# Kernel tuning notes

Hardware: AMD Instinct MI355X
Metric: run time of the kernel (lower is better)

## Reference

```python
import jax, jax.numpy as jnp
import numpy as np

B, N, M, K = 4, 16384, 16384, 16   # batch, points, centers, neighbors
C, O, G = 64, 64, 8                # in_planes, out_planes, group


def setup_inputs() -> dict:
    key = jax.random.key(0)
    ks = jax.random.split(key, 16)
    r = lambda i, sh, s=1.0: jax.random.normal(ks[i], sh, jnp.float32) * s
    return dict(
        center_pos=r(0, (B, M, 3)),
        center_fea=r(1, (B, C, M)),
        pos=r(2, (B, N, 3)),
        fea=r(3, (B, C, N)),
        idx=jax.random.randint(ks[4], (B, M, K), 0, N, jnp.int32),
        # linear q/k/v
        Wq=r(5, (C, O), 0.05), bq=jnp.zeros((O,), jnp.float32),
        Wk=r(6, (C, O), 0.05), bk=jnp.zeros((O,), jnp.float32),
        Wv=r(7, (C, O), 0.05), bv=jnp.zeros((O,), jnp.float32),
        # center_pos_encode: conv1x1(3->O, no bias) + folded BN (scale,shift) + relu + conv1x1(O->O)
        cpe_w1=r(8, (3, O), 0.05), cpe_s=jnp.ones((O,), jnp.float32), cpe_b=jnp.zeros((O,), jnp.float32),
        cpe_w2=r(9, (O, O), 0.05), cpe_b2=jnp.zeros((O,), jnp.float32),
        # pos_encode (Conv2d 1x1 == per-point linear)
        pe_w1=r(10, (3, O), 0.05), pe_s=jnp.ones((O,), jnp.float32), pe_b=jnp.zeros((O,), jnp.float32),
        pe_w2=r(11, (O, O), 0.05), pe_b2=jnp.zeros((O,), jnp.float32),
        # weight_encode (O -> G)
        we_w1=r(12, (O, G), 0.05), we_s=jnp.ones((G,), jnp.float32), we_b=jnp.zeros((G,), jnp.float32),
        we_w2=r(13, (G, G), 0.05), we_b2=jnp.zeros((G,), jnp.float32),
    )


def _mlp2(x, w1, s, b, w2, b2):
    # conv1x1(no bias) -> inference BatchNorm folded to (scale, shift) -> ReLU -> conv1x1(+bias)
    h = jax.nn.relu(x @ w1 * s + b)
    return h @ w2 + b2


def reference(center_pos, center_fea, pos, fea, idx,
              Wq, bq, Wk, bk, Wv, bv,
              cpe_w1, cpe_s, cpe_b, cpe_w2, cpe_b2,
              pe_w1, pe_s, pe_b, pe_w2, pe_b2,
              we_w1, we_s, we_b, we_w2, we_b2):
    x_q = center_fea.transpose(0, 2, 1) @ Wq + bq        # [B,M,O]
    ft = fea.transpose(0, 2, 1)                          # [B,N,C]
    x_k = ft @ Wk + bk                                   # [B,N,O]
    x_v = ft @ Wv + bv                                   # [B,N,O]

    gather = jax.vmap(lambda a, i: a[i])                 # per-batch irregular gather
    nk = gather(x_k, idx)                                # [B,M,K,O]
    nv = gather(x_v, idx)                                # [B,M,K,O]
    npos = gather(pos, idx) - center_pos[:, :, None, :]  # [B,M,K,3] relative coords

    cpr = _mlp2(center_pos, cpe_w1, cpe_s, cpe_b, cpe_w2, cpe_b2)  # [B,M,O]
    pr = _mlp2(npos, pe_w1, pe_s, pe_b, pe_w2, pe_b2)              # [B,M,K,O]

    r_qk = nk - x_q[:, :, None, :] + cpr[:, :, None, :]  # [B,M,K,O]
    v = nv + pr                                          # [B,M,K,O]

    w = _mlp2(r_qk, we_w1, we_s, we_b, we_w2, we_b2)     # [B,M,K,G]
    w = jax.nn.softmax(w, axis=2)                        # softmax over neighbors

    v = v.reshape(B, M, K, G, O // G)
    out = jnp.einsum('bmkgi,bmkg->bmgi', v, w).reshape(B, M, O)
    return out.transpose(0, 2, 1)                        # [B,O,M]
```

## Files before the change

### kernel.cpp

```cpp
#include <hip/hip_runtime.h>
#include <hip/hip_bf16.h>

typedef unsigned short u16;
typedef __attribute__((ext_vector_type(8))) __bf16 bf8v;
typedef __attribute__((ext_vector_type(4))) float f32x4;
typedef __attribute__((ext_vector_type(4))) unsigned uint4v;

#define B_ 4
#define N_ 16384
#define M_ 16384
#define K_ 16
#define C_ 64
#define O_ 64
#define G_ 8

__device__ __forceinline__ float bf2f(u16 x){
  union { unsigned u; float f; } v; v.u = ((unsigned)x) << 16; return v.f;
}
__device__ __forceinline__ u16 f2bf(float f){
  union { float f; unsigned u; } v; v.f = f;
  unsigned u = v.u;
  return (u16)((u + 0x7FFFu + ((u >> 16) & 1u)) >> 16);
}
union pk2 { unsigned u; _Float16 h[2]; };
__device__ __forceinline__ unsigned packh(float a, float b){
  pk2 p; p.h[0] = (_Float16)a; p.h[1] = (_Float16)b; return p.u;
}

__global__ __launch_bounds__(256) void setup_kernel(
    const float* __restrict__ Wq, const float* __restrict__ bq,
    const float* __restrict__ cpe_w2, const float* __restrict__ cpe_b2,
    const float* __restrict__ we_w1,
    const float* __restrict__ Wk, const float* __restrict__ bk,
    const float* __restrict__ Wv, const float* __restrict__ bv,
    const float* __restrict__ cpe_w1, const float* __restrict__ cpe_s, const float* __restrict__ cpe_b,
    u16* __restrict__ bw, float* __restrict__ cinit,
    u16* __restrict__ wkv, float* __restrict__ bias, float* __restrict__ cpe)
{
  __shared__ float sWe[512];
  int tid = threadIdx.x;
  for (int e = tid; e < 512; e += 256) sWe[e] = we_w1[e];
  __syncthreads();
  {
    int k = tid >> 1, g0 = (tid & 1)*4;
    const float* brow = (k < 64) ? (cpe_w2 + k*64) : (Wq + (k-64)*64);
    float sgn = (k < 64) ? 1.f : -1.f;
    float aw[4] = {0.f,0.f,0.f,0.f};
    for (int o = 0; o < 64; o++){
      float bo = brow[o]*sgn;
      #pragma unroll
      for (int gg=0; gg<4; gg++) aw[gg] += bo * sWe[o*8 + g0+gg];
    }
    #pragma unroll
    for (int gg=0; gg<4; gg++) bw[(g0+gg)*136 + k] = f2bf(aw[gg]);
  }
  for (int e = tid; e < 2176; e += 256){
    int r = e / 136, cc = e % 136;
    if (r >= 8 || cc >= 128) bw[e] = 0;
  }
  if (tid < 8){
    float s = 0.f;
    for (int o = 0; o < 64; o++) s += (cpe_b2[o] - bq[o]) * sWe[o*8 + tid];
    cinit[tid] = s;
  }
  for (int e = tid; e < 9216; e += 256){
    int col = e / 72, k = e - col*72;
    float v = 0.f;
    if (k < 64) v = (col < 64) ? Wk[k*64 + col] : Wv[k*64 + (col-64)];
    wkv[e] = f2bf(v);
  }
  if (tid < 128) bias[tid] = (tid < 64) ? bk[tid] : bv[tid-64];
  if (tid < 64){
    float sc = cpe_s[tid];
    cpe[tid]      = cpe_w1[tid]*sc;
    cpe[64+tid]   = cpe_w1[64+tid]*sc;
    cpe[128+tid]  = cpe_w1[128+tid]*sc;
    cpe[192+tid]  = cpe_b[tid];
  }
}

__global__ __launch_bounds__(256) void pre_kernel(
    const float* __restrict__ center_pos, const float* __restrict__ center_fea,
    const float* __restrict__ fea,
    const u16* __restrict__ bw, const float* __restrict__ cinit,
    const u16* __restrict__ wkv, const float* __restrict__ bias, const float* __restrict__ cpe,
    u16* __restrict__ xk, u16* __restrict__ xv, float* __restrict__ qw)
{
  __shared__ u16 sWT[128*72];
  __shared__ u16 sA[64*72];
  __shared__ u16 sOut[64*136];
  __shared__ float sMisc[256];
  int tid = threadIdx.x;
  int l = tid & 63, w = tid >> 6, c = l & 15, q = l >> 4;
  int blk = blockIdx.x;

  if (blk < 256){
    int P0 = blk * 256; int b = P0 >> 14; int n00 = P0 & (N_-1);
    const float* fb = fea + (long)b*C_*N_;
    for (int e = tid; e < 1152; e += 256)
      ((uint4v*)sWT)[e] = ((const uint4v*)wkv)[e];
    if (tid < 128) sMisc[tid] = bias[tid];

    #pragma unroll 1
    for (int s = 0; s < 4; s++){
      int n0 = n00 + s*64;
      #pragma unroll
      for (int pp = 0; pp < 4; pp++){
        int k = pp*16 + (tid >> 4);
        int nf = (tid & 15)*4;
        f32x4 v = *(const f32x4*)&fb[(long)k*N_ + n0 + nf];
        sA[(nf+0)*72+k] = f2bf(v[0]); sA[(nf+1)*72+k] = f2bf(v[1]);
        sA[(nf+2)*72+k] = f2bf(v[2]); sA[(nf+3)*72+k] = f2bf(v[3]);
      }
      __syncthreads();

      bf8v af0 = *(const bf8v*)&sA[(w*16+c)*72 + q*8];
      bf8v af1 = *(const bf8v*)&sA[(w*16+c)*72 + 32 + q*8];
      f32x4 acc[8];
      #pragma unroll
      for (int t = 0; t < 8; t++){
        float bb = sMisc[16*t + c];
        f32x4 a_ = {bb, bb, bb, bb};
        bf8v b0 = *(const bf8v*)&sWT[(16*t + c)*72 + q*8];
        bf8v b1 = *(const bf8v*)&sWT[(16*t + c)*72 + 32 + q*8];
        a_ = __builtin_amdgcn_mfma_f32_16x16x32_bf16(af0, b0, a_, 0,0,0);
        a_ = __builtin_amdgcn_mfma_f32_16x16x32_bf16(af1, b1, a_, 0,0,0);
        acc[t] = a_;
      }
      #pragma unroll
      for (int t = 0; t < 8; t++)
        #pragma unroll
        for (int r = 0; r < 4; r++)
          sOut[(w*16 + q*4 + r)*136 + 16*t + c] = f2bf(acc[t][r]);
      __syncthreads();

      #pragma unroll
      for (int rep = 0; rep < 4; rep++){
        int chunk = rep*256 + tid;
        int pt = chunk >> 4, c8i = chunk & 15;
        uint4v val = *(const uint4v*)&sOut[pt*136 + c8i*8];
        int col8 = c8i*8;
        long row = (long)P0 + s*64 + pt;
        if (col8 < 64) *(uint4v*)(xk + row*64 + col8)      = val;
        else           *(uint4v*)(xv + row*64 + (col8-64)) = val;
      }
      __syncthreads();
    }
  } else {
    int P0 = (blk - 256) * 256; int b = P0 >> 14; int m00 = P0 & (M_-1);
    const float* cfb = center_fea + (long)b*C_*M_;
    float* sQ = (float*)sOut;
    for (int e = tid; e < 272; e += 256)
      ((uint4v*)sWT)[e] = ((const uint4v*)bw)[e];
    if (tid < 256) sMisc[tid] = cpe[tid];

    #pragma unroll 1
    for (int s = 0; s < 4; s++){
      int m0 = m00 + s*64;
      #pragma unroll
      for (int pp = 0; pp < 4; pp++){
        int k = pp*16 + (tid >> 4);
        int nf = (tid & 15)*4;
        f32x4 v = *(const f32x4*)&cfb[(long)k*M_ + m0 + nf];
        sA[(nf+0)*72+k] = f2bf(v[0]); sA[(nf+1)*72+k] = f2bf(v[1]);
        sA[(nf+2)*72+k] = f2bf(v[2]); sA[(nf+3)*72+k] = f2bf(v[3]);
      }
      long c3 = (long)(P0 + s*64 + w*16 + c)*3;
      float cp0 = center_pos[c3], cp1 = center_pos[c3+1], cp2 = center_pos[c3+2];
      __syncthreads();

      bf8v ah[2];
      #pragma unroll
      for (int ks = 0; ks < 2; ks++){
        union { bf8v v; u16 sv[8]; } ua;
        #pragma unroll
        for (int j = 0; j < 8; j++){
          int h = ks*32 + q*8 + j;
          float hv = cp0*sMisc[h] + cp1*sMisc[64+h] + cp2*sMisc[128+h] + sMisc[192+h];
          ua.sv[j] = f2bf(fmaxf(hv, 0.f));
        }
        ah[ks] = ua.v;
      }
      bf8v acf0 = *(const bf8v*)&sA[(w*16+c)*72 + q*8];
      bf8v acf1 = *(const bf8v*)&sA[(w*16+c)*72 + 32 + q*8];

      float ci = (c < 8) ? cinit[c] : 0.f;
      f32x4 aq = {ci, ci, ci, ci};
      {
        bf8v b0 = *(const bf8v*)&sWT[c*136 + q*8];
        bf8v b1 = *(const bf8v*)&sWT[c*136 + 32 + q*8];
        bf8v b2 = *(const bf8v*)&sWT[c*136 + 64 + q*8];
        bf8v b3 = *(const bf8v*)&sWT[c*136 + 96 + q*8];
        aq = __builtin_amdgcn_mfma_f32_16x16x32_bf16(ah[0], b0, aq, 0,0,0);
        aq = __builtin_amdgcn_mfma_f32_16x16x32_bf16(ah[1], b1, aq, 0,0,0);
        aq = __builtin_amdgcn_mfma_f32_16x16x32_bf16(acf0,  b2, aq, 0,0,0);
        aq = __builtin_amdgcn_mfma_f32_16x16x32_bf16(acf1,  b3, aq, 0,0,0);
      }
      __syncthreads();
      if (c < 8){
        #pragma unroll
        for (int r = 0; r < 4; r++) sQ[(w*16 + q*4 + r)*8 + c] = aq[r];
      }
      __syncthreads();
      for (int e = tid; e < 512; e += 256)
        qw[(long)(P0 + s*64)*8 + e] = sQ[e];
      __syncthreads();
    }
  }
}

__global__ __launch_bounds__(256) void attn_kernel(
    const float* __restrict__ center_pos, const float* __restrict__ pos,
    const int* __restrict__ idx,
    const float* __restrict__ pe_w1, const float* __restrict__ pe_s, const float* __restrict__ pe_b,
    const float* __restrict__ pe_w2, const float* __restrict__ pe_b2,
    const float* __restrict__ we_w1, const float* __restrict__ we_s, const float* __restrict__ we_b,
    const float* __restrict__ we_w2, const float* __restrict__ we_b2,
    const u16* __restrict__ xk, const u16* __restrict__ xv, const float* __restrict__ qw,
    float* __restrict__ out)
{
  int tid = threadIdx.x;
  __shared__ float s_w1f[192], s_pb[64], s_pb2[64], s_ww2[64];
  __shared__ float s_ws8[8], s_wb8[8], s_wb28[8];
  __shared__ f32x4 s_dyn4[1232];
  __shared__ float s_tile[32*66];

  char* dynb = (char*)s_dyn4;

  if (tid < 64){
    float sc = pe_s[tid];
    s_w1f[tid]     = pe_w1[tid]*sc;
    s_w1f[64+tid]  = pe_w1[64+tid]*sc;
    s_w1f[128+tid] = pe_w1[128+tid]*sc;
    s_pb[tid]  = pe_b[tid];
    s_pb2[tid] = pe_b2[tid];
    s_ww2[tid] = we_w2[tid];
  }
  if (tid >= 64 && tid < 72){
    int g = tid-64;
    s_ws8[g]=we_s[g]; s_wb8[g]=we_b[g]; s_wb28[g]=we_b2[g];
  }
  u16* stg = (u16*)dynb;
  #pragma unroll
  for (int pp = 0; pp < 4; pp++){
    int row = pp*16 + (tid >> 4);
    int colf = (tid & 15)*4;
    f32x4 v = *(const f32x4*)&pe_w2[row*64 + colf];
    stg[(colf+0)*72+row] = f2bf(v[0]); stg[(colf+1)*72+row] = f2bf(v[1]);
    stg[(colf+2)*72+row] = f2bf(v[2]); stg[(colf+3)*72+row] = f2bf(v[3]);
  }
  u16* stg2 = (u16*)(dynb + 9216);
  for (int e = tid; e < 512; e += 256){
    int k = e >> 3, cc = e & 7;
    stg2[cc*72 + k] = f2bf(we_w1[e]);
  }
  for (int e = tid; e < 576; e += 256) stg2[576 + e] = 0;
  __syncthreads();

  int w = tid >> 6, l = tid & 63, c = l & 15, q = l >> 4, c8 = c & 7, qb = l & 48;

  bf8v pw2f[4][2], ww1f[2], w2B;
  #pragma unroll
  for (int t = 0; t < 4; t++){
    pw2f[t][0] = *(const bf8v*)&stg[(t*16+c)*72 + q*8];
    pw2f[t][1] = *(const bf8v*)&stg[(t*16+c)*72 + 32 + q*8];
  }
  ww1f[0] = *(const bf8v*)&stg2[c*72 + q*8];
  ww1f[1] = *(const bf8v*)&stg2[c*72 + 32 + q*8];
  {
    union { bf8v v; u16 s[8]; } uu;
    #pragma unroll
    for (int j = 0; j < 8; j++)
      uu.s[j] = (q == 0 && c < 8) ? f2bf(s_ww2[j*8 + c]) : (u16)0;
    w2B = uu.v;
  }
  float ws_c = s_ws8[c8], wb_c = s_wb8[c8], wb2_c = s_wb28[c8];
  float pb2l = s_pb2[l];
  __syncthreads();

  float* sv  = (float*)(dynb + w*4928);
  u16*  swt  = (u16*) (dynb + w*4928 + 4352);
  u16*  sh   = (u16*) (dynb + w*4928 + 4672);

  int pbase = blockIdx.x * 32;
  int b = pbase >> 14;
  long xkb = (long)b * N_ * 64;
  int ch = c >> 3;
  int gl = (l >> 3) & 7;

  int p = pbase + w*8;
  int iv = idx[(long)p*16 + c];
  float qpv = qw[(long)p*8 + c8];
  long c30 = (long)p*3;
  float cp0 = center_pos[c30], cp1 = center_pos[c30+1], cp2 = center_pos[c30+2];
  long pr30 = ((long)b*N_ + iv) * 3;
  float px = pos[pr30], py = pos[pr30+1], pz = pos[pr30+2];
  const u16* krow0 = xk + xkb + (long)iv * 64;
  bf8v ka0 = *(const bf8v*)(krow0 + q*8);
  bf8v ka1 = *(const bf8v*)(krow0 + 32 + q*8);
  const u16* vrow0 = xv + xkb + (long)iv * 64;
  uint4v va0 = *(const uint4v*)(vrow0 + q*8);
  uint4v va1 = *(const uint4v*)(vrow0 + 32 + q*8);

  #pragma unroll 1
  for (int i = 0; i < 8; i++){
    int pn = p + ((i < 7) ? 1 : 0);
    int iv_n = idx[(long)pn*16 + c];
    float qpv_n = qw[(long)pn*8 + c8];
    long c3n = (long)pn*3;
    float cpn0 = center_pos[c3n], cpn1 = center_pos[c3n+1], cpn2 = center_pos[c3n+2];
    long pr3n = ((long)b*N_ + iv_n) * 3;
    float pxn = pos[pr3n], pyn = pos[pr3n+1], pzn = pos[pr3n+2];
    const u16* krn = xk + xkb + (long)iv_n * 64;
    bf8v kan0 = *(const bf8v*)(krn + q*8);
    bf8v kan1 = *(const bf8v*)(krn + 32 + q*8);
    const u16* vrn = xv + xkb + (long)iv_n * 64;
    uint4v van0 = *(const uint4v*)(vrn + q*8);
    uint4v van1 = *(const uint4v*)(vrn + 32 + q*8);

    {
      union { uint4v u; u16 s[8]; } A0, A1;
      A0.u = va0; A1.u = va1;
      f32x4 vf0, vf1, vf2, vf3;
      #pragma unroll
      for (int jj = 0; jj < 4; jj++){
        vf0[jj] = bf2f(A0.s[jj]);   vf1[jj] = bf2f(A0.s[4+jj]);
        vf2[jj] = bf2f(A1.s[jj]);   vf3[jj] = bf2f(A1.s[4+jj]);
      }
      f32x4* d0 = (f32x4*)&sv[c*68 + q*8];
      d0[0] = vf0; d0[1] = vf1;
      f32x4* d1 = (f32x4*)&sv[c*68 + 32 + q*8];
      d1[0] = vf2; d1[1] = vf3;
    }

    float np0 = px - cp0, np1 = py - cp1, np2 = pz - cp2;
    bf8v h1f[2];
    #pragma unroll
    for (int ks = 0; ks < 2; ks++){
      union { bf8v v; u16 s[8]; } hu;
      #pragma unroll
      for (int j = 0; j < 8; j++){
        int o = ks*32 + q*8 + j;
        float hv = np0*s_w1f[o] + np1*s_w1f[64+o] + np2*s_w1f[128+o] + s_pb[o];
        hu.s[j] = f2bf(fmaxf(hv, 0.f));
      }
      h1f[ks] = hu.v;
    }

    f32x4 h2a = {qpv, qpv, qpv, qpv};
    h2a = __builtin_amdgcn_mfma_f32_16x16x32_bf16(ka0, ww1f[0], h2a, 0,0,0);
    h2a = __builtin_amdgcn_mfma_f32_16x16x32_bf16(ka1, ww1f[1], h2a, 0,0,0);

    if (c < 8){
      #pragma unroll
      for (int r = 0; r < 4; r++)
        sh[(q*4+r)*8 + c] = f2bf(fmaxf(h2a[r]*ws_c + wb_c, 0.f));
    }
    bf8v hrow = *(const bf8v*)&sh[c*8];
    bf8v zf; { union { bf8v v; u16 s[8]; } uz;
      #pragma unroll
      for (int j=0;j<8;j++) uz.s[j]=0; zf = uz.v; }
    bf8v ahf = (q == 0) ? hrow : zf;

    f32x4 wlv = {wb2_c, wb2_c, wb2_c, wb2_c};
    wlv = __builtin_amdgcn_mfma_f32_16x16x32_bf16(ahf, w2B, wlv, 0,0,0);

    float e0 = exp2f(wlv[0]*1.44269504f);
    float e1 = exp2f(wlv[1]*1.44269504f);
    float e2 = exp2f(wlv[2]*1.44269504f);
    float e3 = exp2f(wlv[3]*1.44269504f);
    float sm = e0+e1+e2+e3;
    sm += __shfl_xor(sm, 16, 64);
    sm += __shfl_xor(sm, 32, 64);
    float rn = 1.0f / sm;
    e0 *= rn; e1 *= rn; e2 *= rn; e3 *= rn;
    unsigned ep0 = packh(e0, e1), ep1 = packh(e2, e3);

    if (c < 8){
      *(unsigned*)&swt[c*20 + q*4]     = ep0;
      *(unsigned*)&swt[c*20 + q*4 + 2] = ep1;
    }

    float ov[4];
    #pragma unroll
    for (int t = 0; t < 4; t++){
      f32x4 z = {0.f,0.f,0.f,0.f};
      z = __builtin_amdgcn_mfma_f32_16x16x32_bf16(h1f[0], pw2f[t][0], z, 0,0,0);
      z = __builtin_amdgcn_mfma_f32_16x16x32_bf16(h1f[1], pw2f[t][1], z, 0,0,0);
      int src = qb | (t*2 + ch);
      pk2 wA; wA.u = (unsigned)__shfl((int)ep0, src, 64);
      pk2 wB; wB.u = (unsigned)__shfl((int)ep1, src, 64);
      ov[t] = z[0]*(float)wA.h[0] + z[1]*(float)wA.h[1]
            + z[2]*(float)wB.h[0] + z[3]*(float)wB.h[1];
    }
    #pragma unroll
    for (int t = 0; t < 4; t++){
      ov[t] += __shfl_xor(ov[t], 16, 64);
      ov[t] += __shfl_xor(ov[t], 32, 64);
    }
    float ovsel = ov[0];
    ovsel = (q==1) ? ov[1] : ovsel;
    ovsel = (q==2) ? ov[2] : ovsel;
    ovsel = (q==3) ? ov[3] : ovsel;

    float acc = 0.f;
    {
      const unsigned* wr = (const unsigned*)&swt[gl*20];
      #pragma unroll
      for (int k2 = 0; k2 < 8; k2++){
        pk2 wp; wp.u = wr[k2];
        acc += sv[(2*k2)*68 + l]   * (float)wp.h[0];
        acc += sv[(2*k2+1)*68 + l] * (float)wp.h[1];
      }
    }

    s_tile[(w*8+i)*66 + l] = ovsel + acc + pb2l;

    p = pn; iv = iv_n; qpv = qpv_n;
    cp0 = cpn0; cp1 = cpn1; cp2 = cpn2;
    px = pxn; py = pyn; pz = pzn;
    ka0 = kan0; ka1 = kan1; va0 = van0; va1 = van1;
  }
  __syncthreads();

  int o0 = tid >> 5, pt = tid & 31;
  int m0 = pbase & (M_-1);
  long outb = ((long)b*64) * M_ + m0 + pt;
  #pragma unroll
  for (int ii = 0; ii < 8; ii++){
    int o = o0*8 + ii;
    out[outb + (long)o*M_] = s_tile[pt*66 + o];
  }
}

extern "C" void kernel_launch(void* const* d_in, const int* in_sizes, int n_in,
                              void* d_out, int out_size, void* d_ws, size_t ws_size,
                              hipStream_t stream) {
  const float* center_pos = (const float*)d_in[0];
  const float* center_fea = (const float*)d_in[1];
  const float* pos        = (const float*)d_in[2];
  const float* fea        = (const float*)d_in[3];
  const int*   idx        = (const int*)d_in[4];
  const float* Wq = (const float*)d_in[5];   const float* bq = (const float*)d_in[6];
  const float* Wk = (const float*)d_in[7];   const float* bk = (const float*)d_in[8];
  const float* Wv = (const float*)d_in[9];   const float* bv = (const float*)d_in[10];
  const float* cpe_w1 = (const float*)d_in[11]; const float* cpe_s = (const float*)d_in[12];
  const float* cpe_b  = (const float*)d_in[13]; const float* cpe_w2 = (const float*)d_in[14];
  const float* cpe_b2 = (const float*)d_in[15];
  const float* pe_w1 = (const float*)d_in[16]; const float* pe_s = (const float*)d_in[17];
  const float* pe_b  = (const float*)d_in[18]; const float* pe_w2 = (const float*)d_in[19];
  const float* pe_b2 = (const float*)d_in[20];
  const float* we_w1 = (const float*)d_in[21]; const float* we_s = (const float*)d_in[22];
  const float* we_b  = (const float*)d_in[23]; const float* we_w2 = (const float*)d_in[24];
  const float* we_b2 = (const float*)d_in[25];

  const size_t SZ = (size_t)B_*N_*64;
  u16* xk = (u16*)d_ws;
  u16* xv = xk + SZ;
  float* qwp = (float*)(xv + SZ);
  u16* bwp = (u16*)(qwp + (size_t)B_*M_*8);
  float* cinitp = (float*)(bwp + 2176);
  u16* wkvp = (u16*)(cinitp + 8);
  float* biasp = (float*)(wkvp + 9216);
  float* cpep = biasp + 128;
  float* outp = (float*)d_out;

  hipLaunchKernelGGL(setup_kernel, dim3(1), dim3(256), 0, stream,
      Wq, bq, cpe_w2, cpe_b2, we_w1, Wk, bk, Wv, bv,
      cpe_w1, cpe_s, cpe_b, bwp, cinitp, wkvp, biasp, cpep);
  hipLaunchKernelGGL(pre_kernel, dim3(512), dim3(256), 0, stream,
      center_pos, center_fea, fea, bwp, cinitp, wkvp, biasp, cpep,
      xk, xv, qwp);
  hipLaunchKernelGGL(attn_kernel, dim3(2048), dim3(256), 0, stream,
      center_pos, pos, idx, pe_w1, pe_s, pe_b, pe_w2, pe_b2,
      we_w1, we_s, we_b, we_w2, we_b2, xk, xv, qwp, outp);
}
```

Before: 229.1 us.

## Fold setup into pre kernel, pad positions to float4, use f16 packed math

Removes the single-block setup kernel and has each pre_kernel block compute its weight transforms (Wk/Wv transpose, folded query/center weights) directly into shared memory. It also writes float4-padded copies of pos and center_pos so the attention kernel can gather positions with one vector load. The attention kernel switches the position-encoding MLP to packed f16 arithmetic and f16 MFMA, and stores softmax weights as f32 in LDS instead of broadcasting them through shuffles. The cost is redundant per-block weight setup, extra LDS and workspace traffic, and different numerical precision in the f16 path.

Result: faster. 207.7 us (-9.3%).

```diff
diff --git a/kernel.cpp b/kernel.cpp
--- a/kernel.cpp
+++ b/kernel.cpp
@@ -3,6 +3,8 @@
 
 typedef unsigned short u16;
 typedef __attribute__((ext_vector_type(8))) __bf16 bf8v;
+typedef __attribute__((ext_vector_type(8))) _Float16 f16x8;
+typedef __attribute__((ext_vector_type(2))) _Float16 h2v;
 typedef __attribute__((ext_vector_type(4))) float f32x4;
 typedef __attribute__((ext_vector_type(4))) unsigned uint4v;
 
@@ -22,74 +24,30 @@
   unsigned u = v.u;
   return (u16)((u + 0x7FFFu + ((u >> 16) & 1u)) >> 16);
 }
-union pk2 { unsigned u; _Float16 h[2]; };
-__device__ __forceinline__ unsigned packh(float a, float b){
-  pk2 p; p.h[0] = (_Float16)a; p.h[1] = (_Float16)b; return p.u;
-}
-
-__global__ __launch_bounds__(256) void setup_kernel(
+__device__ __forceinline__ u16 f2h(float f){
+  union { _Float16 h; u16 u; } v; v.h = (_Float16)f; return v.u;
+}
+__device__ __forceinline__ h2v mkh2(float a, float b){
+  h2v r = {(_Float16)a, (_Float16)b}; return r;
+}
+
+__global__ __launch_bounds__(256) void pre_kernel(
+    const float* __restrict__ center_pos, const float* __restrict__ center_fea,
+    const float* __restrict__ pos, const float* __restrict__ fea,
     const float* __restrict__ Wq, const float* __restrict__ bq,
-    const float* __restrict__ cpe_w2, const float* __restrict__ cpe_b2,
-    const float* __restrict__ we_w1,
     const float* __restrict__ Wk, const float* __restrict__ bk,
     const float* __restrict__ Wv, const float* __restrict__ bv,
     const float* __restrict__ cpe_w1, const float* __restrict__ cpe_s, const float* __restrict__ cpe_b,
-    u16* __restrict__ bw, float* __restrict__ cinit,
-    u16* __restrict__ wkv, float* __restrict__ bias, float* __restrict__ cpe)
-{
-  __shared__ float sWe[512];
-  int tid = threadIdx.x;
-  for (int e = tid; e < 512; e += 256) sWe[e] = we_w1[e];
-  __syncthreads();
-  {
-    int k = tid >> 1, g0 = (tid & 1)*4;
-    const float* brow = (k < 64) ? (cpe_w2 + k*64) : (Wq + (k-64)*64);
-    float sgn = (k < 64) ? 1.f : -1.f;
-    float aw[4] = {0.f,0.f,0.f,0.f};
-    for (int o = 0; o < 64; o++){
-      float bo = brow[o]*sgn;
-      #pragma unroll
-      for (int gg=0; gg<4; gg++) aw[gg] += bo * sWe[o*8 + g0+gg];
-    }
-    #pragma unroll
-    for (int gg=0; gg<4; gg++) bw[(g0+gg)*136 + k] = f2bf(aw[gg]);
-  }
-  for (int e = tid; e < 2176; e += 256){
-    int r = e / 136, cc = e % 136;
-    if (r >= 8 || cc >= 128) bw[e] = 0;
-  }
-  if (tid < 8){
-    float s = 0.f;
-    for (int o = 0; o < 64; o++) s += (cpe_b2[o] - bq[o]) * sWe[o*8 + tid];
-    cinit[tid] = s;
-  }
-  for (int e = tid; e < 9216; e += 256){
-    int col = e / 72, k = e - col*72;
-    float v = 0.f;
-    if (k < 64) v = (col < 64) ? Wk[k*64 + col] : Wv[k*64 + (col-64)];
-    wkv[e] = f2bf(v);
-  }
-  if (tid < 128) bias[tid] = (tid < 64) ? bk[tid] : bv[tid-64];
-  if (tid < 64){
-    float sc = cpe_s[tid];
-    cpe[tid]      = cpe_w1[tid]*sc;
-    cpe[64+tid]   = cpe_w1[64+tid]*sc;
-    cpe[128+tid]  = cpe_w1[128+tid]*sc;
-    cpe[192+tid]  = cpe_b[tid];
-  }
-}
-
-__global__ __launch_bounds__(256) void pre_kernel(
-    const float* __restrict__ center_pos, const float* __restrict__ center_fea,
-    const float* __restrict__ fea,
-    const u16* __restrict__ bw, const float* __restrict__ cinit,
-    const u16* __restrict__ wkv, const float* __restrict__ bias, const float* __restrict__ cpe,
-    u16* __restrict__ xk, u16* __restrict__ xv, float* __restrict__ qw)
+    const float* __restrict__ cpe_w2, const float* __restrict__ cpe_b2,
+    const float* __restrict__ we_w1,
+    u16* __restrict__ xk, u16* __restrict__ xv, float* __restrict__ qw,
+    float* __restrict__ pos4, float* __restrict__ cp4)
 {
   __shared__ u16 sWT[128*72];
   __shared__ u16 sA[64*72];
   __shared__ u16 sOut[64*136];
   __shared__ float sMisc[256];
+  __shared__ float sCi[8];
   int tid = threadIdx.x;
   int l = tid & 63, w = tid >> 6, c = l & 15, q = l >> 4;
   int blk = blockIdx.x;
@@ -97,9 +55,17 @@
   if (blk < 256){
     int P0 = blk * 256; int b = P0 >> 14; int n00 = P0 & (N_-1);
     const float* fb = fea + (long)b*C_*N_;
-    for (int e = tid; e < 1152; e += 256)
-      ((uint4v*)sWT)[e] = ((const uint4v*)wkv)[e];
-    if (tid < 128) sMisc[tid] = bias[tid];
+    for (int e = tid; e < 8192; e += 256){
+      int k = e >> 7, col = e & 127;
+      float v = (col < 64) ? Wk[k*64 + col] : Wv[k*64 + (col-64)];
+      sWT[col*72 + k] = f2bf(v);
+    }
+    if (tid < 128) sMisc[tid] = (tid < 64) ? bk[tid] : bv[tid-64];
+    {
+      long pg = (long)P0 + tid;
+      f32x4 r = {pos[pg*3], pos[pg*3+1], pos[pg*3+2], 0.f};
+      ((f32x4*)pos4)[pg] = r;
+    }
 
     #pragma unroll 1
     for (int s = 0; s < 4; s++){
@@ -149,10 +115,45 @@
   } else {
     int P0 = (blk - 256) * 256; int b = P0 >> 14; int m00 = P0 & (M_-1);
     const float* cfb = center_fea + (long)b*C_*M_;
-    float* sQ = (float*)sOut;
-    for (int e = tid; e < 272; e += 256)
-      ((uint4v*)sWT)[e] = ((const uint4v*)bw)[e];
-    if (tid < 256) sMisc[tid] = cpe[tid];
+    float* sWe = (float*)sOut;
+    float* sQ  = (float*)sOut;
+    for (int e = tid; e < 512; e += 256) sWe[e] = we_w1[e];
+    if (tid < 64){
+      float sc = cpe_s[tid];
+      sMisc[tid]     = cpe_w1[tid]*sc;
+      sMisc[64+tid]  = cpe_w1[64+tid]*sc;
+      sMisc[128+tid] = cpe_w1[128+tid]*sc;
+      sMisc[192+tid] = cpe_b[tid];
+    }
+    {
+      long pg = (long)P0 + tid;
+      f32x4 r = {center_pos[pg*3], center_pos[pg*3+1], center_pos[pg*3+2], 0.f};
+      ((f32x4*)cp4)[pg] = r;
+    }
+    __syncthreads();
+    {
+      int k = tid >> 1, g0 = (tid & 1)*4;
+      const float* brow = (k < 64) ? (cpe_w2 + k*64) : (Wq + (k-64)*64);
+      float sgn = (k < 64) ? 1.f : -1.f;
+      float aw[4] = {0.f,0.f,0.f,0.f};
+      for (int o = 0; o < 64; o++){
+        float bo = brow[o]*sgn;
+        #pragma unroll
+        for (int gg=0; gg<4; gg++) aw[gg] += bo * sWe[o*8 + g0+gg];
+      }
+      #pragma unroll
+      for (int gg=0; gg<4; gg++) sWT[(g0+gg)*136 + k] = f2bf(aw[gg]);
+    }
+    for (int e = tid; e < 2176; e += 256){
+      int r = e / 136, cc = e % 136;
+      if (r >= 8 || cc >= 128) sWT[e] = 0;
+    }
+    if (tid < 8){
+      float s = 0.f;
+      for (int o = 0; o < 64; o++) s += (cpe_b2[o] - bq[o]) * sWe[o*8 + tid];
+      sCi[tid] = s;
+    }
+    __syncthreads();
 
     #pragma unroll 1
     for (int s = 0; s < 4; s++){
@@ -184,7 +185,7 @@
       bf8v acf0 = *(const bf8v*)&sA[(w*16+c)*72 + q*8];
       bf8v acf1 = *(const bf8v*)&sA[(w*16+c)*72 + 32 + q*8];
 
-      float ci = (c < 8) ? cinit[c] : 0.f;
+      float ci = (c < 8) ? sCi[c] : 0.f;
       f32x4 aq = {ci, ci, ci, ci};
       {
         bf8v b0 = *(const bf8v*)&sWT[c*136 + q*8];
@@ -210,7 +211,7 @@
 }
 
 __global__ __launch_bounds__(256) void attn_kernel(
-    const float* __restrict__ center_pos, const float* __restrict__ pos,
+    const float* __restrict__ cp4, const float* __restrict__ pos4,
     const int* __restrict__ idx,
     const float* __restrict__ pe_w1, const float* __restrict__ pe_s, const float* __restrict__ pe_b,
     const float* __restrict__ pe_w2, const float* __restrict__ pe_b2,
@@ -222,7 +223,7 @@
   int tid = threadIdx.x;
   __shared__ float s_w1f[192], s_pb[64], s_pb2[64], s_ww2[64];
   __shared__ float s_ws8[8], s_wb8[8], s_wb28[8];
-  __shared__ f32x4 s_dyn4[1232];
+  __shared__ f32x4 s_dyn4[1312];
   __shared__ float s_tile[32*66];
 
   char* dynb = (char*)s_dyn4;
@@ -246,8 +247,8 @@
     int row = pp*16 + (tid >> 4);
     int colf = (tid & 15)*4;
     f32x4 v = *(const f32x4*)&pe_w2[row*64 + colf];
-    stg[(colf+0)*72+row] = f2bf(v[0]); stg[(colf+1)*72+row] = f2bf(v[1]);
-    stg[(colf+2)*72+row] = f2bf(v[2]); stg[(colf+3)*72+row] = f2bf(v[3]);
+    stg[(colf+0)*72+row] = f2h(v[0]); stg[(colf+1)*72+row] = f2h(v[1]);
+    stg[(colf+2)*72+row] = f2h(v[2]); stg[(colf+3)*72+row] = f2h(v[3]);
   }
   u16* stg2 = (u16*)(dynb + 9216);
   for (int e = tid; e < 512; e += 256){
@@ -259,90 +260,119 @@
 
   int w = tid >> 6, l = tid & 63, c = l & 15, q = l >> 4, c8 = c & 7, qb = l & 48;
 
-  bf8v pw2f[4][2], ww1f[2], w2B;
+  f16x8 pw2f[4][2];
+  bf8v ww1f[2];
+  f16x8 w2B, hz8;
   #pragma unroll
   for (int t = 0; t < 4; t++){
-    pw2f[t][0] = *(const bf8v*)&stg[(t*16+c)*72 + q*8];
-    pw2f[t][1] = *(const bf8v*)&stg[(t*16+c)*72 + 32 + q*8];
+    pw2f[t][0] = *(const f16x8*)&stg[(t*16+c)*72 + q*8];
+    pw2f[t][1] = *(const f16x8*)&stg[(t*16+c)*72 + 32 + q*8];
   }
   ww1f[0] = *(const bf8v*)&stg2[c*72 + q*8];
   ww1f[1] = *(const bf8v*)&stg2[c*72 + 32 + q*8];
   {
-    union { bf8v v; u16 s[8]; } uu;
+    union { f16x8 v; u16 s[8]; } uu;
     #pragma unroll
     for (int j = 0; j < 8; j++)
-      uu.s[j] = (q == 0 && c < 8) ? f2bf(s_ww2[j*8 + c]) : (u16)0;
+      uu.s[j] = (q == 0 && c < 8) ? f2h(s_ww2[j*8 + c]) : (u16)0;
     w2B = uu.v;
-  }
+    #pragma unroll
+    for (int j = 0; j < 8; j++) uu.s[j] = 0;
+    hz8 = uu.v;
+  }
+  h2v cw0[2][4], cw1[2][4], cw2[2][4], cb[2][4];
+  #pragma unroll
+  for (int ks = 0; ks < 2; ks++)
+    #pragma unroll
+    for (int jj = 0; jj < 4; jj++){
+      int o = ks*32 + q*8 + jj*2;
+      cw0[ks][jj] = mkh2(s_w1f[o],     s_w1f[o+1]);
+      cw1[ks][jj] = mkh2(s_w1f[64+o],  s_w1f[65+o]);
+      cw2[ks][jj] = mkh2(s_w1f[128+o], s_w1f[129+o]);
+      cb [ks][jj] = mkh2(s_pb[o],      s_pb[o+1]);
+    }
   float ws_c = s_ws8[c8], wb_c = s_wb8[c8], wb2_c = s_wb28[c8];
   float pb2l = s_pb2[l];
+  h2v hz2 = {(_Float16)0.f, (_Float16)0.f};
   __syncthreads();
 
-  float* sv  = (float*)(dynb + w*4928);
-  u16*  swt  = (u16*) (dynb + w*4928 + 4352);
-  u16*  sh   = (u16*) (dynb + w*4928 + 4672);
+  float* sv  = (float*)(dynb + w*5248);
+  float* swt = (float*)(dynb + w*5248 + 4352);
+  u16*  sh   = (u16*) (dynb + w*5248 + 4992);
 
   int pbase = blockIdx.x * 32;
   int b = pbase >> 14;
-  long xkb = (long)b * N_ * 64;
+  const u16* xkb = xk + (long)b * N_ * 64;
+  const u16* xvb = xv + (long)b * N_ * 64;
+  const f32x4* pos4b = ((const f32x4*)pos4) + (long)b * N_;
   int ch = c >> 3;
-  int gl = (l >> 3) & 7;
-
-  int p = pbase + w*8;
-  int iv = idx[(long)p*16 + c];
-  float qpv = qw[(long)p*8 + c8];
-  long c30 = (long)p*3;
-  float cp0 = center_pos[c30], cp1 = center_pos[c30+1], cp2 = center_pos[c30+2];
-  long pr30 = ((long)b*N_ + iv) * 3;
-  float px = pos[pr30], py = pos[pr30+1], pz = pos[pr30+2];
-  const u16* krow0 = xk + xkb + (long)iv * 64;
-  bf8v ka0 = *(const bf8v*)(krow0 + q*8);
-  bf8v ka1 = *(const bf8v*)(krow0 + 32 + q*8);
-  const u16* vrow0 = xv + xkb + (long)iv * 64;
-  uint4v va0 = *(const uint4v*)(vrow0 + q*8);
-  uint4v va1 = *(const uint4v*)(vrow0 + 32 + q*8);
+  int gl = l >> 3;
+
+  int pb0 = pbase + w*8;
+  const int*   idxl = idx + (long)pb0*16 + c;
+  const float* qwl  = qw  + (long)pb0*8 + c8;
+  const f32x4* cp4l = ((const f32x4*)cp4) + pb0;
+
+  int iv = idxl[0];
+  float qpv = qwl[0];
+  f32x4 cpv = cp4l[0];
+  f32x4 ppv = pos4b[iv];
+  const u16* kr0 = xkb + (size_t)iv*64;
+  bf8v ka0 = *(const bf8v*)(kr0 + q*8);
+  bf8v ka1 = *(const bf8v*)(kr0 + 32 + q*8);
+  const u16* vr0 = xvb + (size_t)iv*64;
+  uint4v va0 = *(const uint4v*)(vr0 + q*8);
+  uint4v va1 = *(const uint4v*)(vr0 + 32 + q*8);
 
   #pragma unroll 1
   for (int i = 0; i < 8; i++){
-    int pn = p + ((i < 7) ? 1 : 0);
-    int iv_n = idx[(long)pn*16 + c];
-    float qpv_n = qw[(long)pn*8 + c8];
-    long c3n = (long)pn*3;
-    float cpn0 = center_pos[c3n], cpn1 = center_pos[c3n+1], cpn2 = center_pos[c3n+2];
-    long pr3n = ((long)b*N_ + iv_n) * 3;
-    float pxn = pos[pr3n], pyn = pos[pr3n+1], pzn = pos[pr3n+2];
-    const u16* krn = xk + xkb + (long)iv_n * 64;
+    int ni = (i < 7) ? i+1 : i;
+    int iv_n = idxl[ni*16];
+    float qpv_n = qwl[ni*8];
+    f32x4 cpn = cp4l[ni];
+    f32x4 ppn = pos4b[iv_n];
+    const u16* krn = xkb + (size_t)iv_n*64;
     bf8v kan0 = *(const bf8v*)(krn + q*8);
     bf8v kan1 = *(const bf8v*)(krn + 32 + q*8);
-    const u16* vrn = xv + xkb + (long)iv_n * 64;
+    const u16* vrn = xvb + (size_t)iv_n*64;
     uint4v van0 = *(const uint4v*)(vrn + q*8);
     uint4v van1 = *(const uint4v*)(vrn + 32 + q*8);
 
     {
-      union { uint4v u; u16 s[8]; } A0, A1;
-      A0.u = va0; A1.u = va1;
-      f32x4 vf0, vf1, vf2, vf3;
+      f32x4 f0, f1, f2, f3;
+      #pragma unroll
+      for (int jj = 0; jj < 2; jj++){
+        unsigned u0 = va0[jj*2], u1 = va0[jj*2+1];
+        f0[jj*2]   = bf2f((u16)u0); f0[jj*2+1] = bf2f((u16)(u0>>16));
+        f1[jj*2]   = bf2f((u16)u1); f1[jj*2+1] = bf2f((u16)(u1>>16));
+      }
+      unsigned a0 = va0[0], a1 = va0[1], a2 = va0[2], a3 = va0[3];
+      f32x4 lo0 = {bf2f((u16)a0), bf2f((u16)(a0>>16)), bf2f((u16)a1), bf2f((u16)(a1>>16))};
+      f32x4 hi0 = {bf2f((u16)a2), bf2f((u16)(a2>>16)), bf2f((u16)a3), bf2f((u16)(a3>>16))};
+      unsigned b0 = va1[0], b1 = va1[1], b2 = va1[2], b3 = va1[3];
+      f32x4 lo1 = {bf2f((u16)b0), bf2f((u16)(b0>>16)), bf2f((u16)b1), bf2f((u16)(b1>>16))};
+      f32x4 hi1 = {bf2f((u16)b2), bf2f((u16)(b2>>16)), bf2f((u16)b3), bf2f((u16)(b3>>16))};
+      f32x4* d0 = (f32x4*)&sv[c*68 + q*8];
+      d0[0] = lo0; d0[1] = hi0;
+      f32x4* d1 = (f32x4*)&sv[c*68 + 32 + q*8];
+      d1[0] = lo1; d1[1] = hi1;
+    }
+
+    float np0 = ppv[0] - cpv[0], np1 = ppv[1] - cpv[1], np2 = ppv[2] - cpv[2];
+    h2v np0h = {(_Float16)np0, (_Float16)np0};
+    h2v np1h = {(_Float16)np1, (_Float16)np1};
+    h2v np2h = {(_Float16)np2, (_Float16)np2};
+    f16x8 h1f[2];
+    #pragma unroll
+    for (int ks = 0; ks < 2; ks++){
+      union { f16x8 v; h2v p[4]; } hu;
       #pragma unroll
       for (int jj = 0; jj < 4; jj++){
-        vf0[jj] = bf2f(A0.s[jj]);   vf1[jj] = bf2f(A0.s[4+jj]);
-        vf2[jj] = bf2f(A1.s[jj]);   vf3[jj] = bf2f(A1.s[4+jj]);
-      }
-      f32x4* d0 = (f32x4*)&sv[c*68 + q*8];
-      d0[0] = vf0; d0[1] = vf1;
-      f32x4* d1 = (f32x4*)&sv[c*68 + 32 + q*8];
-      d1[0] = vf2; d1[1] = vf3;
-    }
-
-    float np0 = px - cp0, np1 = py - cp1, np2 = pz - cp2;
-    bf8v h1f[2];
-    #pragma unroll
-    for (int ks = 0; ks < 2; ks++){
-      union { bf8v v; u16 s[8]; } hu;
-      #pragma unroll
-      for (int j = 0; j < 8; j++){
-        int o = ks*32 + q*8 + j;
-        float hv = np0*s_w1f[o] + np1*s_w1f[64+o] + np2*s_w1f[128+o] + s_pb[o];
-        hu.s[j] = f2bf(fmaxf(hv, 0.f));
+        h2v a = cb[ks][jj];
+        a = np0h*cw0[ks][jj] + a;
+        a = np1h*cw1[ks][jj] + a;
+        a = np2h*cw2[ks][jj] + a;
+        hu.p[jj] = __builtin_elementwise_max(a, hz2);
       }
       h1f[ks] = hu.v;
     }
@@ -354,16 +384,13 @@
     if (c < 8){
       #pragma unroll
       for (int r = 0; r < 4; r++)
-        sh[(q*4+r)*8 + c] = f2bf(fmaxf(h2a[r]*ws_c + wb_c, 0.f));
-    }
-    bf8v hrow = *(const bf8v*)&sh[c*8];
-    bf8v zf; { union { bf8v v; u16 s[8]; } uz;
-      #pragma unroll
-      for (int j=0;j<8;j++) uz.s[j]=0; zf = uz.v; }
-    bf8v ahf = (q == 0) ? hrow : zf;
+        sh[(q*4+r)*8 + c] = f2h(fmaxf(h2a[r]*ws_c + wb_c, 0.f));
+    }
+    f16x8 hrow = *(const f16x8*)&sh[c*8];
+    f16x8 ahf = (q == 0) ? hrow : hz8;
 
     f32x4 wlv = {wb2_c, wb2_c, wb2_c, wb2_c};
-    wlv = __builtin_amdgcn_mfma_f32_16x16x32_bf16(ahf, w2B, wlv, 0,0,0);
+    wlv = __builtin_amdgcn_mfma_f32_16x16x32_f16(ahf, w2B, wlv, 0,0,0);
 
     float e0 = exp2f(wlv[0]*1.44269504f);
     float e1 = exp2f(wlv[1]*1.44269504f);
@@ -373,25 +400,19 @@
     sm += __shfl_xor(sm, 16, 64);
     sm += __shfl_xor(sm, 32, 64);
     float rn = 1.0f / sm;
-    e0 *= rn; e1 *= rn; e2 *= rn; e3 *= rn;
-    unsigned ep0 = packh(e0, e1), ep1 = packh(e2, e3);
-
     if (c < 8){
-      *(unsigned*)&swt[c*20 + q*4]     = ep0;
-      *(unsigned*)&swt[c*20 + q*4 + 2] = ep1;
+      f32x4 ev = {e0*rn, e1*rn, e2*rn, e3*rn};
+      *(f32x4*)&swt[c*20 + q*4] = ev;
     }
 
     float ov[4];
     #pragma unroll
     for (int t = 0; t < 4; t++){
       f32x4 z = {0.f,0.f,0.f,0.f};
-      z = __builtin_amdgcn_mfma_f32_16x16x32_bf16(h1f[0], pw2f[t][0], z, 0,0,0);
-      z = __builtin_amdgcn_mfma_f32_16x16x32_bf16(h1f[1], pw2f[t][1], z, 0,0,0);
-      int src = qb | (t*2 + ch);
-      pk2 wA; wA.u = (unsigned)__shfl((int)ep0, src, 64);
-      pk2 wB; wB.u = (unsigned)__shfl((int)ep1, src, 64);
-      ov[t] = z[0]*(float)wA.h[0] + z[1]*(float)wA.h[1]
-            + z[2]*(float)wB.h[0] + z[3]*(float)wB.h[1];
+      z = __builtin_amdgcn_mfma_f32_16x16x32_f16(h1f[0], pw2f[t][0], z, 0,0,0);
+      z = __builtin_amdgcn_mfma_f32_16x16x32_f16(h1f[1], pw2f[t][1], z, 0,0,0);
+      f32x4 wv = *(const f32x4*)&swt[(t*2+ch)*20 + q*4];
+      ov[t] = z[0]*wv[0] + z[1]*wv[1] + z[2]*wv[2] + z[3]*wv[3];
     }
     #pragma unroll
     for (int t = 0; t < 4; t++){
@@ -403,22 +424,23 @@
     ovsel = (q==2) ? ov[2] : ovsel;
     ovsel = (q==3) ? ov[3] : ovsel;
 
-    float acc = 0.f;
+    float vacc = 0.f;
     {
-      const unsigned* wr = (const unsigned*)&swt[gl*20];
-      #pragma unroll
-      for (int k2 = 0; k2 < 8; k2++){
-        pk2 wp; wp.u = wr[k2];
-        acc += sv[(2*k2)*68 + l]   * (float)wp.h[0];
-        acc += sv[(2*k2+1)*68 + l] * (float)wp.h[1];
-      }
-    }
-
-    s_tile[(w*8+i)*66 + l] = ovsel + acc + pb2l;
-
-    p = pn; iv = iv_n; qpv = qpv_n;
-    cp0 = cpn0; cp1 = cpn1; cp2 = cpn2;
-    px = pxn; py = pyn; pz = pzn;
+      const f32x4* wr4 = (const f32x4*)&swt[gl*20];
+      const float* svl = &sv[l];
+      #pragma unroll
+      for (int k4 = 0; k4 < 4; k4++){
+        f32x4 wv = wr4[k4];
+        vacc += svl[(4*k4+0)*68]*wv[0];
+        vacc += svl[(4*k4+1)*68]*wv[1];
+        vacc += svl[(4*k4+2)*68]*wv[2];
+        vacc += svl[(4*k4+3)*68]*wv[3];
+      }
+    }
+
+    s_tile[(w*8+i)*66 + l] = ovsel + vacc + pb2l;
+
+    iv = iv_n; qpv = qpv_n; cpv = cpn; ppv = ppn;
     ka0 = kan0; ka1 = kan1; va0 = van0; va1 = van1;
   }
   __syncthreads();
@@ -458,20 +480,15 @@
   u16* xk = (u16*)d_ws;
   u16* xv = xk + SZ;
   float* qwp = (float*)(xv + SZ);
-  u16* bwp = (u16*)(qwp + (size_t)B_*M_*8);
-  float* cinitp = (float*)(bwp + 2176);
-  u16* wkvp = (u16*)(cinitp + 8);
-  float* biasp = (float*)(wkvp + 9216);
-  float* cpep = biasp + 128;
+  float* pos4p = qwp + (size_t)B_*M_*8;
+  float* cp4p  = pos4p + (size_t)B_*N_*4;
   float* outp = (float*)d_out;
 
-  hipLaunchKernelGGL(setup_kernel, dim3(1), dim3(256), 0, stream,
-      Wq, bq, cpe_w2, cpe_b2, we_w1, Wk, bk, Wv, bv,
-      cpe_w1, cpe_s, cpe_b, bwp, cinitp, wkvp, biasp, cpep);
   hipLaunchKernelGGL(pre_kernel, dim3(512), dim3(256), 0, stream,
-      center_pos, center_fea, fea, bwp, cinitp, wkvp, biasp, cpep,
-      xk, xv, qwp);
+      center_pos, center_fea, pos, fea, Wq, bq, Wk, bk, Wv, bv,
+      cpe_w1, cpe_s, cpe_b, cpe_w2, cpe_b2, we_w1,
+      xk, xv, qwp, pos4p, cp4p);
   hipLaunchKernelGGL(attn_kernel, dim3(2048), dim3(256), 0, stream,
-      center_pos, pos, idx, pe_w1, pe_s, pe_b, pe_w2, pe_b2,
+      cp4p, pos4p, idx, pe_w1, pe_s, pe_b, pe_w2, pe_b2,
       we_w1, we_s, we_b, we_w2, we_b2, xk, xv, qwp, outp);
 }
```
